# Optimization experiments

Hardware: AMD Instinct MI355X
Metric: run time of the kernel (lower is better)

The kernel has to match this reference:

```python
import jax, jax.numpy as jnp
import numpy as np

N = 50000      # nodes
E = 800000     # edges (avg degree 16)
D_IN, D_H, D_OUT = 128, 256, 128


def setup_inputs() -> dict:
    key = jax.random.key(0)
    ks = jax.random.split(key, 8)
    x = jax.random.normal(ks[0], (N, D_IN), dtype=jnp.float32)
    edge_index = jax.random.randint(ks[1], (2, E), 0, N, dtype=jnp.int64)
    s1 = 1.0 / np.sqrt(D_IN).astype(np.float32)
    s2 = 1.0 / np.sqrt(D_H).astype(np.float32)
    return {
        "x": x,
        "edge_index": edge_index,
        "W1l": jax.random.normal(ks[2], (D_H, D_IN), jnp.float32) * s1,
        "b1l": jnp.zeros((D_H,), jnp.float32),
        "W1r": jax.random.normal(ks[3], (D_H, D_IN), jnp.float32) * s1,
        "W2l": jax.random.normal(ks[4], (D_OUT, D_H), jnp.float32) * s2,
        "b2l": jnp.zeros((D_OUT,), jnp.float32),
        "W2r": jax.random.normal(ks[5], (D_OUT, D_H), jnp.float32) * s2,
    }


def sage_conv(x, src, dst, Wl, bl, Wr):
    # mean-aggregate source features into destination nodes
    agg = jax.ops.segment_sum(x[src], dst, num_segments=N)           # [N, d_in]
    deg = jax.ops.segment_sum(jnp.ones((src.shape[0],), x.dtype), dst, num_segments=N)
    mean = agg / jnp.maximum(deg, 1.0)[:, None]
    # lin_l(mean_agg) + lin_r(x_root); lin_r has no bias (PyG SAGEConv default)
    return mean @ Wl.T + bl + x @ Wr.T


def reference(x, edge_index, W1l, b1l, W1r, W2l, b2l, W2r):
    src, dst = edge_index[0], edge_index[1]
    h = sage_conv(x, src, dst, W1l, b1l, W1r)
    h = jax.nn.relu(h)  # dropout inactive in eval mode
    return sage_conv(h, src, dst, W2l, b2l, W2r)
```

## Files before the change

kernel.cpp:

```cpp
#include <hip/hip_runtime.h>


typedef __attribute__((ext_vector_type(8))) short bf16x8;
typedef __attribute__((ext_vector_type(4))) float floatx4;

__device__ inline unsigned short f2b(float f) {
  unsigned int x = __float_as_uint(f);
  unsigned int r = (x + 0x7fffu + ((x >> 16) & 1u)) >> 16;
  return (unsigned short)r;
}
__device__ inline float blo(unsigned int u) { return __uint_as_float(u << 16); }
__device__ inline float bhi(unsigned int u) { return __uint_as_float(u & 0xffff0000u); }

#define ACC8(A, u)                                            \
  {                                                           \
    A[0] += blo((u).x); A[1] += bhi((u).x);                   \
    A[2] += blo((u).y); A[3] += bhi((u).y);                   \
    A[4] += blo((u).z); A[5] += bhi((u).z);                   \
    A[6] += blo((u).w); A[7] += bhi((u).w);                   \
  }

__global__ void prep_kernel(const float* __restrict__ x,
                            const float* __restrict__ W1l, const float* __restrict__ W1r,
                            const float* __restrict__ W2l, const float* __restrict__ W2r,
                            unsigned short* __restrict__ Wc1, unsigned short* __restrict__ Wc2,
                            unsigned short* __restrict__ A1,
                            int* __restrict__ cnt, int* __restrict__ off, int N, int E) {
  int i = blockIdx.x * blockDim.x + threadIdx.x;
  if (i < 65536) {
    int j = i >> 8, k = i & 255;
    float v1 = (k < 128) ? W1l[j * 128 + k] : W1r[j * 128 + (k - 128)];
    Wc1[i] = f2b(v1);
    float v2 = (j < 128) ? W2l[j * 256 + k] : W2r[(j - 128) * 256 + k];
    Wc2[i] = f2b(v2);
  }
  if (i < N) cnt[i] = 0;
  if (i == 0) off[N] = E;
  if (i < N * 32) {
    int n = i >> 5, c = (i & 31) * 4;
    float4 v = *(const float4*)(x + (size_t)n * 128 + c);
    uint2 p;
    p.x = (unsigned int)f2b(v.x) | ((unsigned int)f2b(v.y) << 16);
    p.y = (unsigned int)f2b(v.z) | ((unsigned int)f2b(v.w) << 16);
    *(uint2*)(A1 + (size_t)n * 256 + 128 + c) = p;
  }
}

__global__ void hist_kernel(const int* __restrict__ dst, int* __restrict__ cnt,
                            int* __restrict__ rank, int E) {
  int i = blockIdx.x * blockDim.x + threadIdx.x;
  int e = i * 4;
  if (e + 3 < E) {
    int4 d = *(const int4*)(dst + e);
    int4 r;
    r.x = atomicAdd(&cnt[d.x], 1);
    r.y = atomicAdd(&cnt[d.y], 1);
    r.z = atomicAdd(&cnt[d.z], 1);
    r.w = atomicAdd(&cnt[d.w], 1);
    *(int4*)(rank + e) = r;
  } else {
    for (; e < E; e++) rank[e] = atomicAdd(&cnt[dst[e]], 1);
  }
}

__global__ __launch_bounds__(1024) void scan_blocks_kernel(const int* __restrict__ cnt,
                                                           int* __restrict__ off,
                                                           int* __restrict__ bsum, int N) {
  __shared__ int wsum[16];
  __shared__ int wincl[16];
  const int tid = threadIdx.x;
  const int lane = tid & 63;
  const int wv = tid >> 6;
  const int i = blockIdx.x * 1024 + tid;
  const int v = (i < N) ? cnt[i] : 0;
  int s = v;
#pragma unroll
  for (int o = 1; o < 64; o <<= 1) {
    int t = __shfl_up(s, o, 64);
    if (lane >= o) s += t;
  }
  if (lane == 63) wsum[wv] = s;
  __syncthreads();
  if (tid < 16) {
    int ws = wsum[tid];
#pragma unroll
    for (int o = 1; o < 16; o <<= 1) {
      int t = __shfl_up(ws, o, 16);
      if ((tid & 15) >= o) ws += t;
    }
    wincl[tid] = ws;
  }
  __syncthreads();
  const int wo = wv ? wincl[wv - 1] : 0;
  if (i < N) off[i] = wo + s - v;
  if (tid == 1023) bsum[blockIdx.x] = wo + s;
}

__global__ __launch_bounds__(1024) void scan_add_kernel(int* __restrict__ off,
                                                        const int* __restrict__ bsum, int N, int SB) {
  __shared__ int bofs[64];
  const int tid = threadIdx.x;
  if (tid < 64) {
    int v = (tid < SB) ? bsum[tid] : 0;
    int s = v;
#pragma unroll
    for (int o = 1; o < 64; o <<= 1) {
      int t = __shfl_up(s, o, 64);
      if (tid >= o) s += t;
    }
    bofs[tid] = s - v;
  }
  __syncthreads();
  int i = blockIdx.x * 1024 + tid;
  if (i < N) off[i] = off[i] + bofs[blockIdx.x];
}

__global__ void fill_kernel(const int* __restrict__ src, const int* __restrict__ dst,
                            const int* __restrict__ rank, const int* __restrict__ off,
                            int* __restrict__ csr, int E) {
  int i = blockIdx.x * blockDim.x + threadIdx.x;
  int e = i * 4;
  if (e + 3 < E) {
    int4 d = *(const int4*)(dst + e);
    int4 r = *(const int4*)(rank + e);
    int4 s = *(const int4*)(src + e);
    csr[off[d.x] + r.x] = s.x;
    csr[off[d.y] + r.y] = s.y;
    csr[off[d.z] + r.z] = s.z;
    csr[off[d.w] + r.w] = s.w;
  } else {
    for (; e < E; e++) csr[off[dst[e]] + rank[e]] = src[e];
  }
}

__global__ void gather1_kernel(const unsigned short* __restrict__ feat,
                               const int* __restrict__ csr, const int* __restrict__ off,
                               unsigned short* __restrict__ ob, int N) {
  int wid = (blockIdx.x * blockDim.x + threadIdx.x) >> 6;
  if (wid >= N) return;
  const int lane = threadIdx.x & 63;
  const int slot = lane >> 3;
  const int j = lane & 7;
  const int c0 = j * 8;
  const int s0 = off[wid], s1 = off[wid + 1];
  float a[16] = {};
  int e = s0 + slot;
  for (; e + 8 < s1; e += 16) {
    int i0 = csr[e], i1 = csr[e + 8];
    uint4 u0 = *(const uint4*)(feat + (size_t)i0 * 256 + c0);
    uint4 v0 = *(const uint4*)(feat + (size_t)i0 * 256 + 64 + c0);
    uint4 u1 = *(const uint4*)(feat + (size_t)i1 * 256 + c0);
    uint4 v1 = *(const uint4*)(feat + (size_t)i1 * 256 + 64 + c0);
    ACC8(a, u0); ACC8((a + 8), v0);
    ACC8(a, u1); ACC8((a + 8), v1);
  }
  for (; e < s1; e += 8) {
    int i0 = csr[e];
    uint4 u0 = *(const uint4*)(feat + (size_t)i0 * 256 + c0);
    uint4 v0 = *(const uint4*)(feat + (size_t)i0 * 256 + 64 + c0);
    ACC8(a, u0); ACC8((a + 8), v0);
  }
#pragma unroll
  for (int k = 0; k < 16; k++) {
    a[k] += __shfl_xor(a[k], 8, 64);
    a[k] += __shfl_xor(a[k], 16, 64);
    a[k] += __shfl_xor(a[k], 32, 64);
  }
  if (slot == 0) {
    const float inv = 1.0f / fmaxf((float)(s1 - s0), 1.0f);
    uint4 p;
    p.x = (unsigned int)f2b(a[0] * inv) | ((unsigned int)f2b(a[1] * inv) << 16);
    p.y = (unsigned int)f2b(a[2] * inv) | ((unsigned int)f2b(a[3] * inv) << 16);
    p.z = (unsigned int)f2b(a[4] * inv) | ((unsigned int)f2b(a[5] * inv) << 16);
    p.w = (unsigned int)f2b(a[6] * inv) | ((unsigned int)f2b(a[7] * inv) << 16);
    *(uint4*)(ob + (size_t)wid * 256 + c0) = p;
    p.x = (unsigned int)f2b(a[8] * inv) | ((unsigned int)f2b(a[9] * inv) << 16);
    p.y = (unsigned int)f2b(a[10] * inv) | ((unsigned int)f2b(a[11] * inv) << 16);
    p.z = (unsigned int)f2b(a[12] * inv) | ((unsigned int)f2b(a[13] * inv) << 16);
    p.w = (unsigned int)f2b(a[14] * inv) | ((unsigned int)f2b(a[15] * inv) << 16);
    *(uint4*)(ob + (size_t)wid * 256 + 64 + c0) = p;
  }
}

__global__ void gather2_kernel(const unsigned short* __restrict__ t,
                               const int* __restrict__ csr, const int* __restrict__ off,
                               float* __restrict__ out, int N) {
  int wid = (blockIdx.x * blockDim.x + threadIdx.x) >> 6;
  if (wid >= N) return;
  const int lane = threadIdx.x & 63;
  const int slot = lane >> 3;
  const int j = lane & 7;
  const int c0 = j * 8;
  const int s0 = off[wid], s1 = off[wid + 1];
  float a[16] = {};
  int e = s0 + slot;
  for (; e + 8 < s1; e += 16) {
    int i0 = csr[e], i1 = csr[e + 8];
    uint4 u0 = *(const uint4*)(t + (size_t)i0 * 128 + c0);
    uint4 v0 = *(const uint4*)(t + (size_t)i0 * 128 + 64 + c0);
    uint4 u1 = *(const uint4*)(t + (size_t)i1 * 128 + c0);
    uint4 v1 = *(const uint4*)(t + (size_t)i1 * 128 + 64 + c0);
    ACC8(a, u0); ACC8((a + 8), v0);
    ACC8(a, u1); ACC8((a + 8), v1);
  }
  for (; e < s1; e += 8) {
    int i0 = csr[e];
    uint4 u0 = *(const uint4*)(t + (size_t)i0 * 128 + c0);
    uint4 v0 = *(const uint4*)(t + (size_t)i0 * 128 + 64 + c0);
    ACC8(a, u0); ACC8((a + 8), v0);
  }
#pragma unroll
  for (int k = 0; k < 16; k++) {
    a[k] += __shfl_xor(a[k], 8, 64);
    a[k] += __shfl_xor(a[k], 16, 64);
    a[k] += __shfl_xor(a[k], 32, 64);
  }
  if (slot == 0) {
    const float inv = 1.0f / fmaxf((float)(s1 - s0), 1.0f);
    float4* o0 = (float4*)(out + (size_t)wid * 128 + c0);
    float4* o1 = (float4*)(out + (size_t)wid * 128 + 64 + c0);
    float4 r0 = o0[0], r1 = o0[1], r2 = o1[0], r3 = o1[1];
    r0.x += a[0] * inv;  r0.y += a[1] * inv;  r0.z += a[2] * inv;  r0.w += a[3] * inv;
    r1.x += a[4] * inv;  r1.y += a[5] * inv;  r1.z += a[6] * inv;  r1.w += a[7] * inv;
    r2.x += a[8] * inv;  r2.y += a[9] * inv;  r2.z += a[10] * inv; r2.w += a[11] * inv;
    r3.x += a[12] * inv; r3.y += a[13] * inv; r3.z += a[14] * inv; r3.w += a[15] * inv;
    o0[0] = r0; o0[1] = r1; o1[0] = r2; o1[1] = r3;
  }
}

__global__ __launch_bounds__(256, 4)
void gemm_fused(const unsigned short* __restrict__ A,
                const unsigned short* __restrict__ Wc1,
                const unsigned short* __restrict__ Wc2,
                const float* __restrict__ b1, const float* __restrict__ b2,
                unsigned short* __restrict__ tb, float* __restrict__ out, int M) {
  constexpr int LDH = 264;
  __shared__ __align__(16) unsigned short Hs[64 * LDH];
  const int t = threadIdx.x;
  const int lane = t & 63;
  const int wave = t >> 6;
  const int wn = wave * 64;
  const int l15 = lane & 15;
  const int quad = lane >> 4;
  const int m_blk = blockIdx.x * 64;

  const unsigned short* ap[4];
  const unsigned short* wp[4];
#pragma unroll
  for (int mt = 0; mt < 4; mt++) {
    int ar = m_blk + mt * 16 + l15;
    if (ar >= M) ar = M - 1;
    ap[mt] = A + (size_t)ar * 256 + quad * 8;
  }
#pragma unroll
  for (int nt = 0; nt < 4; nt++)
    wp[nt] = Wc1 + (size_t)(wn + nt * 16 + l15) * 256 + quad * 8;

  floatx4 acc[4][4] = {};

#pragma unroll 2
  for (int ks = 0; ks < 256; ks += 32) {
    bf16x8 af[4], bfr[4];
#pragma unroll
    for (int mt = 0; mt < 4; mt++) af[mt] = *(const bf16x8*)(ap[mt] + ks);
#pragma unroll
    for (int nt = 0; nt < 4; nt++) bfr[nt] = *(const bf16x8*)(wp[nt] + ks);
#pragma unroll
    for (int mt = 0; mt < 4; mt++)
#pragma unroll
      for (int nt = 0; nt < 4; nt++)
        acc[mt][nt] = __builtin_amdgcn_mfma_f32_16x16x32_bf16(af[mt], bfr[nt], acc[mt][nt], 0, 0, 0);
  }

#pragma unroll
  for (int nt = 0; nt < 4; nt++) {
    const int jl = wn + nt * 16 + l15;
    const float bv = b1[jl];
#pragma unroll
    for (int mt = 0; mt < 4; mt++) {
#pragma unroll
      for (int r = 0; r < 4; r++) {
        const int row = mt * 16 + quad * 4 + r;
        Hs[row * LDH + jl] = f2b(fmaxf(acc[mt][nt][r] + bv, 0.f));
      }
    }
  }
  __syncthreads();

#pragma unroll
  for (int mt = 0; mt < 4; mt++)
#pragma unroll
    for (int nt = 0; nt < 4; nt++)
      acc[mt][nt] = (floatx4){0.f, 0.f, 0.f, 0.f};
#pragma unroll
  for (int nt = 0; nt < 4; nt++)
    wp[nt] = Wc2 + (size_t)(wn + nt * 16 + l15) * 256 + quad * 8;
  const unsigned short* hp0 = Hs + l15 * LDH + quad * 8;

#pragma unroll 2
  for (int ks = 0; ks < 256; ks += 32) {
    bf16x8 af[4], bfr[4];
#pragma unroll
    for (int mt = 0; mt < 4; mt++)
      af[mt] = *(const bf16x8*)(hp0 + mt * 16 * LDH + ks);
#pragma unroll
    for (int nt = 0; nt < 4; nt++) bfr[nt] = *(const bf16x8*)(wp[nt] + ks);
#pragma unroll
    for (int mt = 0; mt < 4; mt++)
#pragma unroll
      for (int nt = 0; nt < 4; nt++)
        acc[mt][nt] = __builtin_amdgcn_mfma_f32_16x16x32_bf16(af[mt], bfr[nt], acc[mt][nt], 0, 0, 0);
  }

#pragma unroll
  for (int nt = 0; nt < 4; nt++) {
    const int j = wn + nt * 16 + l15;
#pragma unroll
    for (int mt = 0; mt < 4; mt++) {
#pragma unroll
      for (int r = 0; r < 4; r++) {
        const int node = m_blk + mt * 16 + quad * 4 + r;
        if (node >= M) continue;
        const float v = acc[mt][nt][r];
        if (j < 128) {
          tb[(size_t)node * 128 + j] = f2b(v);
        } else {
          out[(size_t)node * 128 + (j - 128)] = v + b2[j - 128];
        }
      }
    }
  }
}

extern "C" void kernel_launch(void* const* d_in, const int* in_sizes, int n_in,
                              void* d_out, int out_size, void* d_ws, size_t ws_size,
                              hipStream_t stream) {
  const float* x   = (const float*)d_in[0];
  const int*  eidx = (const int*)d_in[1];
  const float* W1l = (const float*)d_in[2];
  const float* b1l = (const float*)d_in[3];
  const float* W1r = (const float*)d_in[4];
  const float* W2l = (const float*)d_in[5];
  const float* b2l = (const float*)d_in[6];
  const float* W2r = (const float*)d_in[7];
  float* out = (float*)d_out;

  const int N = in_sizes[0] / 128;
  const int E = in_sizes[1] / 2;
  const int* src = eidx;
  const int* dst = eidx + E;

  int* cnt  = (int*)d_ws;
  int* off  = cnt + N;
  int* bsum = off + N + 1;
  int* rank = bsum + 64;
  int* csr  = rank + E;
  size_t ioff = ((size_t)(N + N + 1 + 64 + 2 * E) * 4 + 15) & ~(size_t)15;
  unsigned short* A1  = (unsigned short*)((char*)d_ws + ioff);
  unsigned short* tb  = A1 + (size_t)N * 256;
  unsigned short* Wc1 = tb + (size_t)N * 128;
  unsigned short* Wc2 = Wc1 + 65536;

  const int SB = (N + 1023) / 1024;

  prep_kernel<<<(N * 32 + 255) / 256, 256, 0, stream>>>(x, W1l, W1r, W2l, W2r,
                                                        Wc1, Wc2, A1, cnt, off, N, E);
  hist_kernel<<<(E / 4 + 255) / 256, 256, 0, stream>>>(dst, cnt, rank, E);
  scan_blocks_kernel<<<SB, 1024, 0, stream>>>(cnt, off, bsum, N);
  scan_add_kernel<<<SB, 1024, 0, stream>>>(off, bsum, N, SB);
  fill_kernel<<<(E / 4 + 255) / 256, 256, 0, stream>>>(src, dst, rank, off, csr, E);

  const int gblocks = (N + 3) / 4;
  gather1_kernel<<<gblocks, 256, 0, stream>>>(A1 + 128, csr, off, A1, N);

  gemm_fused<<<(N + 63) / 64, 256, 0, stream>>>(A1, Wc1, Wc2, b1l, b2l, tb, out, N);

  gather2_kernel<<<gblocks, 256, 0, stream>>>(tb, csr, off, out, N);
}
```

Baseline: 282.1 us.

## Split fused GEMM into two kernels with LDS-staged A and register-resident weights

Replaces the single fused two-layer GEMM kernel with two separate kernels, each using 512 threads. Each wave keeps its 32-column weight slice in registers, and the A tile is staged once into LDS. The intermediate hidden activation H now round-trips through global memory as bf16, which adds about 25 MB each of writes and reads. In exchange the weight-fragment global loads leave the k-loop, and each GEMM can run at higher occupancy.

```diff
diff --git a/kernel.cpp b/kernel.cpp
--- a/kernel.cpp
+++ b/kernel.cpp
@@ -228,95 +228,122 @@
   }
 }
 
-__global__ __launch_bounds__(256, 4)
-void gemm_fused(const unsigned short* __restrict__ A,
-                const unsigned short* __restrict__ Wc1,
-                const unsigned short* __restrict__ Wc2,
-                const float* __restrict__ b1, const float* __restrict__ b2,
-                unsigned short* __restrict__ tb, float* __restrict__ out, int M) {
-  constexpr int LDH = 264;
-  __shared__ __align__(16) unsigned short Hs[64 * LDH];
+__global__ __launch_bounds__(512, 4)
+void gemm1(const unsigned short* __restrict__ A, const unsigned short* __restrict__ Wc1,
+           const float* __restrict__ b1, unsigned short* __restrict__ H, int M) {
+  constexpr int LDA = 264;
+  __shared__ __align__(16) unsigned short As[64 * LDA];
   const int t = threadIdx.x;
   const int lane = t & 63;
   const int wave = t >> 6;
-  const int wn = wave * 64;
+  const int wn = wave * 32;
   const int l15 = lane & 15;
   const int quad = lane >> 4;
   const int m_blk = blockIdx.x * 64;
 
-  const unsigned short* ap[4];
-  const unsigned short* wp[4];
+  bf16x8 wr[2][8];
+#pragma unroll
+  for (int nt = 0; nt < 2; nt++) {
+    const unsigned short* wp = Wc1 + (size_t)(wn + nt * 16 + l15) * 256 + quad * 8;
+#pragma unroll
+    for (int c = 0; c < 8; c++) wr[nt][c] = *(const bf16x8*)(wp + c * 32);
+  }
+  const float bv0 = b1[wn + l15];
+  const float bv1 = b1[wn + 16 + l15];
+
+#pragma unroll
+  for (int i = 0; i < 4; i++) {
+    int idx = t + 512 * i;
+    int row = idx >> 5, cc = (idx & 31) * 8;
+    int ar = m_blk + row;
+    if (ar >= M) ar = M - 1;
+    *(uint4*)(As + row * LDA + cc) = *(const uint4*)(A + (size_t)ar * 256 + cc);
+  }
+  __syncthreads();
+
+  floatx4 acc[4][2] = {};
+#pragma unroll
+  for (int c = 0; c < 8; c++) {
+    bf16x8 af[4];
+#pragma unroll
+    for (int mt = 0; mt < 4; mt++)
+      af[mt] = *(const bf16x8*)(As + (mt * 16 + l15) * LDA + c * 32 + quad * 8);
+#pragma unroll
+    for (int mt = 0; mt < 4; mt++) {
+      acc[mt][0] = __builtin_amdgcn_mfma_f32_16x16x32_bf16(af[mt], wr[0][c], acc[mt][0], 0, 0, 0);
+      acc[mt][1] = __builtin_amdgcn_mfma_f32_16x16x32_bf16(af[mt], wr[1][c], acc[mt][1], 0, 0, 0);
+    }
+  }
+
 #pragma unroll
   for (int mt = 0; mt < 4; mt++) {
-    int ar = m_blk + mt * 16 + l15;
+#pragma unroll
+    for (int nt = 0; nt < 2; nt++) {
+      const int j = wn + nt * 16 + l15;
+      const float bv = nt ? bv1 : bv0;
+#pragma unroll
+      for (int r = 0; r < 4; r++) {
+        const int node = m_blk + mt * 16 + quad * 4 + r;
+        if (node < M) H[(size_t)node * 256 + j] = f2b(fmaxf(acc[mt][nt][r] + bv, 0.f));
+      }
+    }
+  }
+}
+
+__global__ __launch_bounds__(512, 4)
+void gemm2(const unsigned short* __restrict__ H, const unsigned short* __restrict__ Wc2,
+           const float* __restrict__ b2, unsigned short* __restrict__ tb,
+           float* __restrict__ out, int M) {
+  constexpr int LDA = 264;
+  __shared__ __align__(16) unsigned short As[64 * LDA];
+  const int t = threadIdx.x;
+  const int lane = t & 63;
+  const int wave = t >> 6;
+  const int wn = wave * 32;
+  const int l15 = lane & 15;
+  const int quad = lane >> 4;
+  const int m_blk = blockIdx.x * 64;
+
+  bf16x8 wr[2][8];
+#pragma unroll
+  for (int nt = 0; nt < 2; nt++) {
+    const unsigned short* wp = Wc2 + (size_t)(wn + nt * 16 + l15) * 256 + quad * 8;
+#pragma unroll
+    for (int c = 0; c < 8; c++) wr[nt][c] = *(const bf16x8*)(wp + c * 32);
+  }
+  const float bv0 = (wn >= 128) ? b2[wn - 128 + l15] : 0.f;
+  const float bv1 = (wn >= 128) ? b2[wn - 112 + l15] : 0.f;
+
+#pragma unroll
+  for (int i = 0; i < 4; i++) {
+    int idx = t + 512 * i;
+    int row = idx >> 5, cc = (idx & 31) * 8;
+    int ar = m_blk + row;
     if (ar >= M) ar = M - 1;
-    ap[mt] = A + (size_t)ar * 256 + quad * 8;
-  }
-#pragma unroll
-  for (int nt = 0; nt < 4; nt++)
-    wp[nt] = Wc1 + (size_t)(wn + nt * 16 + l15) * 256 + quad * 8;
-
-  floatx4 acc[4][4] = {};
-
-#pragma unroll 2
-  for (int ks = 0; ks < 256; ks += 32) {
-    bf16x8 af[4], bfr[4];
-#pragma unroll
-    for (int mt = 0; mt < 4; mt++) af[mt] = *(const bf16x8*)(ap[mt] + ks);
-#pragma unroll
-    for (int nt = 0; nt < 4; nt++) bfr[nt] = *(const bf16x8*)(wp[nt] + ks);
+    *(uint4*)(As + row * LDA + cc) = *(const uint4*)(H + (size_t)ar * 256 + cc);
+  }
+  __syncthreads();
+
+  floatx4 acc[4][2] = {};
+#pragma unroll
+  for (int c = 0; c < 8; c++) {
+    bf16x8 af[4];
 #pragma unroll
     for (int mt = 0; mt < 4; mt++)
-#pragma unroll
-      for (int nt = 0; nt < 4; nt++)
-        acc[mt][nt] = __builtin_amdgcn_mfma_f32_16x16x32_bf16(af[mt], bfr[nt], acc[mt][nt], 0, 0, 0);
-  }
-
-#pragma unroll
-  for (int nt = 0; nt < 4; nt++) {
-    const int jl = wn + nt * 16 + l15;
-    const float bv = b1[jl];
+      af[mt] = *(const bf16x8*)(As + (mt * 16 + l15) * LDA + c * 32 + quad * 8);
 #pragma unroll
     for (int mt = 0; mt < 4; mt++) {
-#pragma unroll
-      for (int r = 0; r < 4; r++) {
-        const int row = mt * 16 + quad * 4 + r;
-        Hs[row * LDH + jl] = f2b(fmaxf(acc[mt][nt][r] + bv, 0.f));
-      }
-    }
-  }
-  __syncthreads();
-
-#pragma unroll
-  for (int mt = 0; mt < 4; mt++)
-#pragma unroll
-    for (int nt = 0; nt < 4; nt++)
-      acc[mt][nt] = (floatx4){0.f, 0.f, 0.f, 0.f};
-#pragma unroll
-  for (int nt = 0; nt < 4; nt++)
-    wp[nt] = Wc2 + (size_t)(wn + nt * 16 + l15) * 256 + quad * 8;
-  const unsigned short* hp0 = Hs + l15 * LDH + quad * 8;
-
-#pragma unroll 2
-  for (int ks = 0; ks < 256; ks += 32) {
-    bf16x8 af[4], bfr[4];
-#pragma unroll
-    for (int mt = 0; mt < 4; mt++)
-      af[mt] = *(const bf16x8*)(hp0 + mt * 16 * LDH + ks);
-#pragma unroll
-    for (int nt = 0; nt < 4; nt++) bfr[nt] = *(const bf16x8*)(wp[nt] + ks);
-#pragma unroll
-    for (int mt = 0; mt < 4; mt++)
-#pragma unroll
-      for (int nt = 0; nt < 4; nt++)
-        acc[mt][nt] = __builtin_amdgcn_mfma_f32_16x16x32_bf16(af[mt], bfr[nt], acc[mt][nt], 0, 0, 0);
-  }
-
-#pragma unroll
-  for (int nt = 0; nt < 4; nt++) {
-    const int j = wn + nt * 16 + l15;
-#pragma unroll
-    for (int mt = 0; mt < 4; mt++) {
+      acc[mt][0] = __builtin_amdgcn_mfma_f32_16x16x32_bf16(af[mt], wr[0][c], acc[mt][0], 0, 0, 0);
+      acc[mt][1] = __builtin_amdgcn_mfma_f32_16x16x32_bf16(af[mt], wr[1][c], acc[mt][1], 0, 0, 0);
+    }
+  }
+
+#pragma unroll
+  for (int mt = 0; mt < 4; mt++) {
+#pragma unroll
+    for (int nt = 0; nt < 2; nt++) {
+      const int j = wn + nt * 16 + l15;
+      const float bv = nt ? bv1 : bv0;
 #pragma unroll
       for (int r = 0; r < 4; r++) {
         const int node = m_blk + mt * 16 + quad * 4 + r;
@@ -325,7 +352,7 @@
         if (j < 128) {
           tb[(size_t)node * 128 + j] = f2b(v);
         } else {
-          out[(size_t)node * 128 + (j - 128)] = v + b2[j - 128];
+          out[(size_t)node * 128 + (j - 128)] = v + bv;
         }
       }
     }
@@ -357,7 +384,8 @@
   int* csr  = rank + E;
   size_t ioff = ((size_t)(N + N + 1 + 64 + 2 * E) * 4 + 15) & ~(size_t)15;
   unsigned short* A1  = (unsigned short*)((char*)d_ws + ioff);
-  unsigned short* tb  = A1 + (size_t)N * 256;
+  unsigned short* h   = A1 + (size_t)N * 256;
+  unsigned short* tb  = h + (size_t)N * 256;
   unsigned short* Wc1 = tb + (size_t)N * 128;
   unsigned short* Wc2 = Wc1 + 65536;
 
@@ -373,7 +401,9 @@
   const int gblocks = (N + 3) / 4;
   gather1_kernel<<<gblocks, 256, 0, stream>>>(A1 + 128, csr, off, A1, N);
 
-  gemm_fused<<<(N + 63) / 64, 256, 0, stream>>>(A1, Wc1, Wc2, b1l, b2l, tb, out, N);
+  const int mblocks = (N + 63) / 64;
+  gemm1<<<mblocks, 512, 0, stream>>>(A1, Wc1, b1l, h, N);
+  gemm2<<<mblocks, 512, 0, stream>>>(h, Wc2, b2l, tb, out, N);
 
   gather2_kernel<<<gblocks, 256, 0, stream>>>(tb, csr, off, out, N);
 }
```

Result: faster. 275.8 us (-2.2%).
